# Kernel optimization log

Measured on AMD Instinct MI355X. Metric: run time of the kernel, lower is better.

Reference implementation:

```python
import jax, jax.numpy as jnp
import numpy as np

ITERS = 10  # resonator iterations (iterations=10 in init_kwargs)

def _bipolar(key, shape):
    return jnp.where(jax.random.normal(key, shape) >= 0, 1.0, -1.0).astype(jnp.float32)

def setup_inputs() -> dict:
    key = jax.random.key(0)
    k1, k2, k3 = jax.random.split(key, 3)
    b, f, v, d = 64, 4, 256, 16384
    input_ = _bipolar(k1, (b, d))
    init_estimates = _bipolar(k2, (b, f, d))
    codebooks = _bipolar(k3, (f, v, d))
    return {"input": input_, "init_estimates": init_estimates, "codebooks": codebooks}

def _sign(x):
    # multiset quantize: bipolar sign (ties -> +1), matching MAP-VSA quantization
    return jnp.where(x >= 0, 1.0, -1.0).astype(x.dtype)

def reference(input, init_estimates, codebooks):
    """CONCURRENT resonator, SOFTWARE mode, activation=NONE, stoch=NONE.
    input: (b, d) bipolar; init_estimates: (b, f, d); codebooks: (f, v, d).
    For bipolar vectors: bind = elementwise *, inverse = identity, so
    multibind of all-but-factor-j equals (product over all f) * estimate_j
    (since e*e = 1). This replaces the roll+stack+multibind with one fused pass.
    """
    def step(est, _):
        total = jnp.prod(est, axis=-2, keepdims=True)        # (b, 1, d)
        inv_others = total * est                             # (b, f, d) product of other factors
        new_est = input[:, None, :] * inv_others             # unbind: (b, f, d)
        sim = jnp.einsum('bfd,fvd->bfv', new_est, codebooks) # dot_similarity
        # multiset(codebook, similarity, quantize=True): sign of similarity-weighted sum
        est_new = _sign(jnp.einsum('bfv,fvd->bfd', sim, codebooks))
        return est_new, None
    est, _ = jax.lax.scan(step, init_estimates, None, length=ITERS)
    # cleanup: argmax of |similarity| per factor (argmax_abs=True)
    sim = jnp.einsum('bfd,fvd->bfv', est, codebooks)
    outcome = jnp.argmax(jnp.abs(sim), axis=-1)              # (b, f) codeword indices
    return est, outcome
```

## Files before the change

kernel.cpp:

```cpp
#include <hip/hip_runtime.h>
#include <stdint.h>

typedef unsigned long long ull;
typedef unsigned short ushort_t;
typedef __attribute__((ext_vector_type(8))) short bf16x8;
typedef __attribute__((ext_vector_type(4))) float f32x4;


__global__ __launch_bounds__(1024) void pack_mega(
        const float* __restrict__ in, const float* __restrict__ est_f,
        const float* __restrict__ cb,
        ull* __restrict__ in_bits, ull* __restrict__ est_bits, ull* __restrict__ cbw) {
    int wid  = (int)((blockIdx.x * 1024 + threadIdx.x) >> 6);
    int lane = threadIdx.x & 63;
    int w0 = wid * 16;
    const float* s;
    int wloc;
    if (w0 < 16384)      { s = in;    wloc = w0; }
    else if (w0 < 81920) { s = est_f; wloc = w0 - 16384; }
    else                 { s = cb;    wloc = w0 - 81920; }
    ull ball[16];
    #pragma unroll
    for (int k = 0; k < 16; ++k) {
        float x = s[(size_t)(wloc + k) * 64 + lane];
        ball[k] = __ballot(x < 0.0f);
    }
    if (lane == 0) {
        if (w0 < 16384) {
            #pragma unroll
            for (int k = 0; k < 16; ++k) in_bits[wloc + k] = ball[k];
        } else if (w0 < 81920) {
            #pragma unroll
            for (int k = 0; k < 16; ++k) est_bits[wloc + k] = ball[k];
        } else {
            #pragma unroll
            for (int k = 0; k < 16; ++k) {
                int g = wloc + k;
                int f = g >> 16, v = (g >> 8) & 255, w = g & 255;
                cbw[(size_t)(f * 256 + w) * 256 + v] = ball[k];
            }
        }
    }
}

__global__ __launch_bounds__(1024) void pack_cbT(const ull* __restrict__ cbw, ull* __restrict__ cbT) {
    int wid  = (int)((blockIdx.x * 1024 + threadIdx.x) >> 6);
    int lane = threadIdx.x & 63;
    int f = wid >> 12, j = (wid >> 10) & 3, w = (wid >> 2) & 255, s2 = wid & 3;
    ull cw = cbw[(size_t)(f * 256 + w) * 256 + j * 64 + lane];
    ull ball[16];
    #pragma unroll
    for (int k = 0; k < 16; ++k)
        ball[k] = __ballot((cw >> (s2 * 16 + k)) & 1ull);
    if (lane == 0) {
        #pragma unroll
        for (int k = 0; k < 16; ++k)
            cbT[(size_t)(f * 4 + j) * 16384 + w * 64 + s2 * 16 + k] = ball[k];
    }
}

__global__ __launch_bounds__(1024) void simA3_kernel(
        const ull* __restrict__ in_bits, const ull* __restrict__ est_in,
        const ull* __restrict__ cbw, ushort_t* __restrict__ outq, int mode) {
    int bid = blockIdx.x;
    int f    = (bid & 7) >> 1;
    int sub  = (bid & 1) * 32 + (bid >> 3);
    int vblk = sub & 3, bblk = sub >> 2;

    __shared__ ull s_cw[256][64];
    __shared__ ull s_ne[4][256];
    __shared__ short s_p[4][4][64];

    int t = threadIdx.x;

    {
        int bl = t >> 8, w = t & 255;
        int b = bblk * 4 + bl;
        ull e0 = est_in[(size_t)(b * 4 + 0) * 256 + w];
        ull e1 = est_in[(size_t)(b * 4 + 1) * 256 + w];
        ull e2 = est_in[(size_t)(b * 4 + 2) * 256 + w];
        ull e3 = est_in[(size_t)(b * 4 + 3) * 256 + w];
        ull ef = (f == 0) ? e0 : ((f == 1) ? e1 : ((f == 2) ? e2 : e3));
        s_ne[bl][w] = mode ? ef
                           : (in_bits[(size_t)b * 256 + w] ^ e0 ^ e1 ^ e2 ^ e3 ^ ef);
    }
    #pragma unroll 4
    for (int i = 0; i < 16; ++i) {
        int idx = i * 1024 + t;
        int w = idx >> 6, v = idx & 63;
        s_cw[w][v] = cbw[(size_t)(f * 256 + w) * 256 + vblk * 64 + v];
    }
    __syncthreads();

    {
        int lane = t & 63, wave = t >> 6;
        int bi = wave & 3, q = wave >> 2;
        int acc = 0;
        #pragma unroll 8
        for (int w = q * 64; w < q * 64 + 64; ++w)
            acc += __popcll(s_ne[bi][w] ^ s_cw[w][lane]);
        s_p[bi][q][lane] = (short)acc;
    }
    __syncthreads();

    if (t < 256) {
        int bi = t >> 6, v2 = t & 63;
        int h = s_p[bi][0][v2] + s_p[bi][1][v2] + s_p[bi][2][v2] + s_p[bi][3][v2];
        int b = bblk * 4 + bi, v = vblk * 64 + v2;
        if (mode == 0) {
            int sim = 16384 - 2 * h;
            int sh = sim >> 8, sl = sim & 255;
            size_t base = ((size_t)(f * 64 + b)) * 512 + v;
            outq[base]       = (ushort_t)(__float_as_uint((float)sh) >> 16);
            outq[base + 256] = (ushort_t)(__float_as_uint((float)sl) >> 16);
        } else {
            outq[((size_t)(f * 64 + b)) * 256 + v] = (ushort_t)(16384 - h);
        }
    }
}

__global__ __launch_bounds__(512) void gemm_kernel(
        const ull* __restrict__ cbT, const ushort_t* __restrict__ simAB,
        ull* __restrict__ est_out) {
    int bid = blockIdx.x;
    int fB   = (bid & 7) >> 1;
    int dblk = (bid & 1) * 32 + (bid >> 3);
    __shared__ int4 sB[8192];
    __shared__ ull s_ball[8][8][4];
    int t = threadIdx.x, lane = t & 63, wave = t >> 6;

    #pragma unroll 4
    for (int it = 0; it < 16; ++it) {
        int flat = it * 512 + t;
        int kc = flat >> 10, nt = (flat >> 6) & 15, l = flat & 63;
        int v0 = kc * 32 + ((l >> 4) << 3);
        int d  = dblk * 256 + nt * 16 + (l & 15);
        ull w = cbT[((size_t)fB * 4 + (v0 >> 6)) * 16384 + d];
        unsigned bits = (unsigned)(w >> (v0 & 63)) & 0xFFu;
        int4 val;
        val.x = 0x3F803F80 | ((bits & 1u) << 15)        | ((bits & 2u) << 30);
        val.y = 0x3F803F80 | (((bits >> 2) & 1u) << 15) | (((bits >> 2) & 2u) << 30);
        val.z = 0x3F803F80 | (((bits >> 4) & 1u) << 15) | (((bits >> 4) & 2u) << 30);
        val.w = 0x3F803F80 | (((bits >> 6) & 1u) << 15) | (((bits >> 6) & 2u) << 30);
        sB[flat] = val;
    }

    int mw = wave & 3, ntb = (wave >> 2) << 3;
    const ushort_t* abase = simAB
        + ((size_t)(fB * 64 + mw * 16 + (lane & 15))) * 512 + ((lane >> 4) << 3);
    bf16x8 Ahi[8], Alo[8];
    #pragma unroll
    for (int kc = 0; kc < 8; ++kc) {
        Ahi[kc] = *(const bf16x8*)(abase + kc * 32);
        Alo[kc] = *(const bf16x8*)(abase + 256 + kc * 32);
    }
    __syncthreads();

    #pragma unroll 2
    for (int ntl = 0; ntl < 8; ++ntl) {
        int nt = ntb + ntl;
        f32x4 acch = {0.f, 0.f, 0.f, 0.f}, accl = {0.f, 0.f, 0.f, 0.f};
        #pragma unroll
        for (int kc = 0; kc < 8; ++kc) {
            bf16x8 B = *(const bf16x8*)&sB[(kc * 16 + nt) * 64 + lane];
            acch = __builtin_amdgcn_mfma_f32_16x16x32_bf16(Ahi[kc], B, acch, 0, 0, 0);
            accl = __builtin_amdgcn_mfma_f32_16x16x32_bf16(Alo[kc], B, accl, 0, 0, 0);
        }
        #pragma unroll
        for (int r = 0; r < 4; ++r) {
            float S = 256.0f * acch[r] + accl[r];
            ull m = __ballot(S < 0.0f);
            if (lane == 0) s_ball[wave][nt & 7][r] = m;
        }
    }
    __syncthreads();

    if (t < 256) {
        int b = t >> 2, w4 = t & 3;
        int wv = (b >> 4) + ((w4 >= 2) ? 4 : 0);
        ull word = 0;
        #pragma unroll
        for (int k = 0; k < 4; ++k) {
            int nt = w4 * 4 + k;
            ull m = s_ball[wv][nt & 7][b & 3];
            word |= ((m >> (((b >> 2) & 3) * 16)) & 0xFFFFull) << (k * 16);
        }
        est_out[((size_t)(b * 4 + fB)) * 256 + dblk * 4 + w4] = word;
    }
}

__global__ __launch_bounds__(256) void final2_kernel(
        const ull* __restrict__ est, const ushort_t* __restrict__ simF,
        float* __restrict__ out) {
    int t = threadIdx.x;
    if (blockIdx.x < 256 && t < 64) {
        int b = blockIdx.x >> 2, f = blockIdx.x & 3;
        const ushort_t* sf = simF + ((size_t)(f * 64 + b)) * 256 + t * 4;
        int best_a = -1, best_v = 0;
        #pragma unroll
        for (int k = 0; k < 4; ++k) {
            int sim = 2 * (int)sf[k] - 16384;
            int a = sim < 0 ? -sim : sim;
            if (a > best_a) { best_a = a; best_v = t * 4 + k; }
        }
        #pragma unroll
        for (int off = 1; off < 64; off <<= 1) {
            int oa = __shfl_xor(best_a, off);
            int ov = __shfl_xor(best_v, off);
            if (oa > best_a || (oa == best_a && ov < best_v)) { best_a = oa; best_v = ov; }
        }
        if (t == 0) out[4194304 + b * 4 + f] = (float)best_v;
    }
    int flat = blockIdx.x * 2048 + t * 8;
    ull w = est[flat >> 6];
    unsigned bits = (unsigned)(w >> (flat & 63)) & 0xFFu;
    float4 lo, hi;
    lo.x = (bits & 1u)   ? -1.0f : 1.0f;
    lo.y = (bits & 2u)   ? -1.0f : 1.0f;
    lo.z = (bits & 4u)   ? -1.0f : 1.0f;
    lo.w = (bits & 8u)   ? -1.0f : 1.0f;
    hi.x = (bits & 16u)  ? -1.0f : 1.0f;
    hi.y = (bits & 32u)  ? -1.0f : 1.0f;
    hi.z = (bits & 64u)  ? -1.0f : 1.0f;
    hi.w = (bits & 128u) ? -1.0f : 1.0f;
    *(float4*)(out + flat)     = lo;
    *(float4*)(out + flat + 4) = hi;
}

extern "C" void kernel_launch(void* const* d_in, const int* in_sizes, int n_in,
                              void* d_out, int out_size, void* d_ws, size_t ws_size,
                              hipStream_t stream) {
    const float* input    = (const float*)d_in[0];
    const float* init_est = (const float*)d_in[1];
    const float* cb       = (const float*)d_in[2];
    float* out = (float*)d_out;
    char* ws = (char*)d_ws;

    ull* in_bits    = (ull*)(ws + 0);
    ull* est0       = (ull*)(ws + 131072);
    ull* est1       = (ull*)(ws + 655360);
    ull* cbw        = (ull*)(ws + 1179648);
    ull* cbT        = (ull*)(ws + 3276800);
    ushort_t* simAB = (ushort_t*)(ws + 5373952);
    ushort_t* simF  = simAB;

    pack_mega<<<1344, 1024, 0, stream>>>(input, init_est, cb, in_bits, est0, cbw);
    pack_cbT<<<1024, 1024, 0, stream>>>(cbw, cbT);

    ull* bufs[2] = { est0, est1 };
    for (int i = 0; i < 10; ++i) {
        simA3_kernel<<<256, 1024, 0, stream>>>(in_bits, bufs[i & 1], cbw, simAB, 0);
        gemm_kernel<<<256, 512, 0, stream>>>(cbT, simAB, bufs[(i & 1) ^ 1]);
    }
    simA3_kernel<<<256, 1024, 0, stream>>>(in_bits, est0, cbw, simF, 1);
    final2_kernel<<<2048, 256, 0, stream>>>(est0, simF, out);
}
```

Before: 318.9 us.

## Fuse resonator iterations into one persistent cooperative kernel with grid barriers

Replaces the 22 separate similarity/GEMM/final kernel launches with a single cooperative persistent kernel of 256 blocks. Blocks synchronise through atomic counters in global memory, and shared memory is reused between the popcount and MFMA phases. It also overlaps codebook staging into shared memory with the barrier waits. This removes launch overhead and inter-kernel gaps, at the cost of spin-wait barriers and reloading codebook tiles every iteration because the shared buffer is aliased.

```diff
diff --git a/kernel.cpp b/kernel.cpp
--- a/kernel.cpp
+++ b/kernel.cpp
@@ -2,15 +2,31 @@
 #include <stdint.h>
 
 typedef unsigned long long ull;
-typedef unsigned short ushort_t;
+typedef unsigned int u32;
 typedef __attribute__((ext_vector_type(8))) short bf16x8;
 typedef __attribute__((ext_vector_type(4))) float f32x4;
 
+
+#define AS __HIP_MEMORY_SCOPE_AGENT
+__device__ __forceinline__ ull ald(const ull* p) {
+    return __hip_atomic_load(p, __ATOMIC_RELAXED, AS);
+}
+__device__ __forceinline__ void ast(ull* p, ull v) {
+    __hip_atomic_store(p, v, __ATOMIC_RELAXED, AS);
+}
+__device__ __forceinline__ u32 ald32(const u32* p) {
+    return __hip_atomic_load(p, __ATOMIC_RELAXED, AS);
+}
+__device__ __forceinline__ void ast32(u32* p, u32 v) {
+    __hip_atomic_store(p, v, __ATOMIC_RELAXED, AS);
+}
 
 __global__ __launch_bounds__(1024) void pack_mega(
         const float* __restrict__ in, const float* __restrict__ est_f,
         const float* __restrict__ cb,
-        ull* __restrict__ in_bits, ull* __restrict__ est_bits, ull* __restrict__ cbw) {
+        ull* __restrict__ in_bits, ull* __restrict__ est_bits, ull* __restrict__ cbw,
+        ull* __restrict__ bar) {
+    if (blockIdx.x == 0 && threadIdx.x < 64) bar[threadIdx.x] = 0;
     int wid  = (int)((blockIdx.x * 1024 + threadIdx.x) >> 6);
     int lane = threadIdx.x & 63;
     int w0 = wid * 16;
@@ -59,147 +75,174 @@
     }
 }
 
-__global__ __launch_bounds__(1024) void simA3_kernel(
-        const ull* __restrict__ in_bits, const ull* __restrict__ est_in,
-        const ull* __restrict__ cbw, ushort_t* __restrict__ outq, int mode) {
+__global__ __launch_bounds__(512) void reso_kernel(
+        const ull* __restrict__ in_bits, ull* __restrict__ est0, ull* __restrict__ est1,
+        const ull* __restrict__ cbw, const ull* __restrict__ cbT,
+        u32* __restrict__ simAB, ull* __restrict__ bar, float* __restrict__ out) {
+    __shared__ __align__(16) char smraw[143360];
+    ull  (*s_cw)[64]     = (ull (*)[64])smraw;
+    ull  (*s_ne)[256]    = (ull (*)[256])(smraw + 131072);
+    short (*s_p)[8][64]  = (short (*)[8][64])(smraw + 139264);
+    int4* sB             = (int4*)smraw;
+    ull  (*s_ball)[8][4] = (ull (*)[8][4])(smraw + 131072);
+
+    int t = threadIdx.x, lane = t & 63, wave = t >> 6;
     int bid = blockIdx.x;
     int f    = (bid & 7) >> 1;
     int sub  = (bid & 1) * 32 + (bid >> 3);
     int vblk = sub & 3, bblk = sub >> 2;
-
-    __shared__ ull s_cw[256][64];
-    __shared__ ull s_ne[4][256];
-    __shared__ short s_p[4][4][64];
-
-    int t = threadIdx.x;
-
-    {
-        int bl = t >> 8, w = t & 255;
-        int b = bblk * 4 + bl;
-        ull e0 = est_in[(size_t)(b * 4 + 0) * 256 + w];
-        ull e1 = est_in[(size_t)(b * 4 + 1) * 256 + w];
-        ull e2 = est_in[(size_t)(b * 4 + 2) * 256 + w];
-        ull e3 = est_in[(size_t)(b * 4 + 3) * 256 + w];
-        ull ef = (f == 0) ? e0 : ((f == 1) ? e1 : ((f == 2) ? e2 : e3));
-        s_ne[bl][w] = mode ? ef
-                           : (in_bits[(size_t)b * 256 + w] ^ e0 ^ e1 ^ e2 ^ e3 ^ ef);
-    }
+    int dblk = sub;
+
     #pragma unroll 4
     for (int i = 0; i < 16; ++i) {
-        int idx = i * 1024 + t;
+        int idx = i * 1024 + t * 2;
         int w = idx >> 6, v = idx & 63;
-        s_cw[w][v] = cbw[(size_t)(f * 256 + w) * 256 + vblk * 64 + v];
-    }
-    __syncthreads();
-
-    {
-        int lane = t & 63, wave = t >> 6;
-        int bi = wave & 3, q = wave >> 2;
-        int acc = 0;
-        #pragma unroll 8
-        for (int w = q * 64; w < q * 64 + 64; ++w)
-            acc += __popcll(s_ne[bi][w] ^ s_cw[w][lane]);
-        s_p[bi][q][lane] = (short)acc;
-    }
-    __syncthreads();
-
-    if (t < 256) {
-        int bi = t >> 6, v2 = t & 63;
-        int h = s_p[bi][0][v2] + s_p[bi][1][v2] + s_p[bi][2][v2] + s_p[bi][3][v2];
-        int b = bblk * 4 + bi, v = vblk * 64 + v2;
-        if (mode == 0) {
-            int sim = 16384 - 2 * h;
-            int sh = sim >> 8, sl = sim & 255;
-            size_t base = ((size_t)(f * 64 + b)) * 512 + v;
-            outq[base]       = (ushort_t)(__float_as_uint((float)sh) >> 16);
-            outq[base + 256] = (ushort_t)(__float_as_uint((float)sl) >> 16);
-        } else {
-            outq[((size_t)(f * 64 + b)) * 256 + v] = (ushort_t)(16384 - h);
-        }
-    }
-}
-
-__global__ __launch_bounds__(512) void gemm_kernel(
-        const ull* __restrict__ cbT, const ushort_t* __restrict__ simAB,
-        ull* __restrict__ est_out) {
-    int bid = blockIdx.x;
-    int fB   = (bid & 7) >> 1;
-    int dblk = (bid & 1) * 32 + (bid >> 3);
-    __shared__ int4 sB[8192];
-    __shared__ ull s_ball[8][8][4];
-    int t = threadIdx.x, lane = t & 63, wave = t >> 6;
-
-    #pragma unroll 4
-    for (int it = 0; it < 16; ++it) {
-        int flat = it * 512 + t;
-        int kc = flat >> 10, nt = (flat >> 6) & 15, l = flat & 63;
-        int v0 = kc * 32 + ((l >> 4) << 3);
-        int d  = dblk * 256 + nt * 16 + (l & 15);
-        ull w = cbT[((size_t)fB * 4 + (v0 >> 6)) * 16384 + d];
-        unsigned bits = (unsigned)(w >> (v0 & 63)) & 0xFFu;
-        int4 val;
-        val.x = 0x3F803F80 | ((bits & 1u) << 15)        | ((bits & 2u) << 30);
-        val.y = 0x3F803F80 | (((bits >> 2) & 1u) << 15) | (((bits >> 2) & 2u) << 30);
-        val.z = 0x3F803F80 | (((bits >> 4) & 1u) << 15) | (((bits >> 4) & 2u) << 30);
-        val.w = 0x3F803F80 | (((bits >> 6) & 1u) << 15) | (((bits >> 6) & 2u) << 30);
-        sB[flat] = val;
-    }
-
-    int mw = wave & 3, ntb = (wave >> 2) << 3;
-    const ushort_t* abase = simAB
-        + ((size_t)(fB * 64 + mw * 16 + (lane & 15))) * 512 + ((lane >> 4) << 3);
-    bf16x8 Ahi[8], Alo[8];
-    #pragma unroll
-    for (int kc = 0; kc < 8; ++kc) {
-        Ahi[kc] = *(const bf16x8*)(abase + kc * 32);
-        Alo[kc] = *(const bf16x8*)(abase + 256 + kc * 32);
-    }
-    __syncthreads();
-
-    #pragma unroll 2
-    for (int ntl = 0; ntl < 8; ++ntl) {
-        int nt = ntb + ntl;
-        f32x4 acch = {0.f, 0.f, 0.f, 0.f}, accl = {0.f, 0.f, 0.f, 0.f};
+        *(ulonglong2*)&s_cw[w][v] =
+            *(const ulonglong2*)&cbw[(size_t)(f * 256 + w) * 256 + vblk * 64 + v];
+    }
+
+    for (int itr = 0; itr <= 10; ++itr) {
+        ull* estIn  = (itr & 1) ? est1 : est0;
+        ull* estOut = (itr & 1) ? est0 : est1;
+        const int mode = (itr == 10);
+
+        #pragma unroll
+        for (int i = 0; i < 2; ++i) {
+            int idx = i * 512 + t;
+            int bl = idx >> 8, w = idx & 255;
+            int b = bblk * 4 + bl;
+            ull e0 = ald(&estIn[(size_t)(b * 4 + 0) * 256 + w]);
+            ull e1 = ald(&estIn[(size_t)(b * 4 + 1) * 256 + w]);
+            ull e2 = ald(&estIn[(size_t)(b * 4 + 2) * 256 + w]);
+            ull e3 = ald(&estIn[(size_t)(b * 4 + 3) * 256 + w]);
+            ull ef = (f == 0) ? e0 : ((f == 1) ? e1 : ((f == 2) ? e2 : e3));
+            s_ne[bl][w] = mode ? ef : (in_bits[(size_t)b * 256 + w] ^ e0 ^ e1 ^ e2 ^ e3 ^ ef);
+        }
+        __syncthreads();
+        {
+            int acc0 = 0, acc1 = 0, acc2 = 0, acc3 = 0;
+            #pragma unroll 8
+            for (int w = wave * 32; w < wave * 32 + 32; ++w) {
+                ull cwv = s_cw[w][lane];
+                acc0 += __popcll(s_ne[0][w] ^ cwv);
+                acc1 += __popcll(s_ne[1][w] ^ cwv);
+                acc2 += __popcll(s_ne[2][w] ^ cwv);
+                acc3 += __popcll(s_ne[3][w] ^ cwv);
+            }
+            s_p[0][wave][lane] = (short)acc0;
+            s_p[1][wave][lane] = (short)acc1;
+            s_p[2][wave][lane] = (short)acc2;
+            s_p[3][wave][lane] = (short)acc3;
+        }
+        __syncthreads();
+        if (t < 256) {
+            int bi = t >> 6, v2 = t & 63;
+            int h = 0;
+            #pragma unroll
+            for (int c = 0; c < 8; ++c) h += s_p[bi][c][v2];
+            int b = bblk * 4 + bi, v = vblk * 64 + v2;
+            u32 val;
+            if (!mode) {
+                int sim = 16384 - 2 * h;
+                int sh = sim >> 8, sl = sim & 255;
+                val = (u32)(__float_as_uint((float)sh) >> 16)
+                    | ((u32)(__float_as_uint((float)sl) >> 16) << 16);
+            } else {
+                val = (u32)(16384 - h);
+            }
+            ast32(&simAB[((size_t)(f * 64 + b) << 8) + v], val);
+        }
+        __syncthreads();
+        if (t == 0) atomicAdd(&bar[itr * 2], 1ull);
+        if (!mode) {
+            #pragma unroll 4
+            for (int it2 = 0; it2 < 16; ++it2) {
+                int flat = it2 * 512 + t;
+                int kc = flat >> 10, nt = (flat >> 6) & 15, l = flat & 63;
+                int v0 = kc * 32 + ((l >> 4) << 3);
+                int d  = dblk * 256 + nt * 16 + (l & 15);
+                ull w = cbT[((size_t)f * 4 + (v0 >> 6)) * 16384 + d];
+                unsigned bits = (unsigned)(w >> (v0 & 63)) & 0xFFu;
+                int4 valB;
+                valB.x = 0x3F803F80 | ((bits & 1u) << 15)        | ((bits & 2u) << 30);
+                valB.y = 0x3F803F80 | (((bits >> 2) & 1u) << 15) | (((bits >> 2) & 2u) << 30);
+                valB.z = 0x3F803F80 | (((bits >> 4) & 1u) << 15) | (((bits >> 4) & 2u) << 30);
+                valB.w = 0x3F803F80 | (((bits >> 6) & 1u) << 15) | (((bits >> 6) & 2u) << 30);
+                sB[flat] = valB;
+            }
+        }
+        if (t == 0) { while (ald(&bar[itr * 2]) < 256ull) __builtin_amdgcn_s_sleep(1); }
+        __syncthreads();
+        if (mode) break;
+
+        int mw = wave & 3, ntb = (wave >> 2) << 3;
+        const ull* ab = (const ull*)(simAB + (((size_t)(f * 64 + mw * 16 + (lane & 15))) << 8))
+                        + ((lane >> 4) << 2);
+        bf16x8 Ahi[8], Alo[8];
         #pragma unroll
         for (int kc = 0; kc < 8; ++kc) {
-            bf16x8 B = *(const bf16x8*)&sB[(kc * 16 + nt) * 64 + lane];
-            acch = __builtin_amdgcn_mfma_f32_16x16x32_bf16(Ahi[kc], B, acch, 0, 0, 0);
-            accl = __builtin_amdgcn_mfma_f32_16x16x32_bf16(Alo[kc], B, accl, 0, 0, 0);
-        }
-        #pragma unroll
-        for (int r = 0; r < 4; ++r) {
-            float S = 256.0f * acch[r] + accl[r];
-            ull m = __ballot(S < 0.0f);
-            if (lane == 0) s_ball[wave][nt & 7][r] = m;
-        }
-    }
-    __syncthreads();
-
-    if (t < 256) {
-        int b = t >> 2, w4 = t & 3;
-        int wv = (b >> 4) + ((w4 >= 2) ? 4 : 0);
-        ull word = 0;
+            union { u32 u[4]; bf16x8 v; } H, L;
+            #pragma unroll
+            for (int p2 = 0; p2 < 4; ++p2) {
+                ull w = ald(ab + kc * 16 + p2);
+                H.u[p2] = (u32)(w & 0xFFFFull) | (((u32)(w >> 32) & 0xFFFFu) << 16);
+                L.u[p2] = ((u32)(w >> 16) & 0xFFFFu) | ((u32)(w >> 48) << 16);
+            }
+            Ahi[kc] = H.v; Alo[kc] = L.v;
+        }
+        #pragma unroll 2
+        for (int ntl = 0; ntl < 8; ++ntl) {
+            int nt = ntb + ntl;
+            f32x4 acch = {0.f, 0.f, 0.f, 0.f}, accl = {0.f, 0.f, 0.f, 0.f};
+            #pragma unroll
+            for (int kc = 0; kc < 8; ++kc) {
+                bf16x8 B = *(const bf16x8*)&sB[(kc * 16 + nt) * 64 + lane];
+                acch = __builtin_amdgcn_mfma_f32_16x16x32_bf16(Ahi[kc], B, acch, 0, 0, 0);
+                accl = __builtin_amdgcn_mfma_f32_16x16x32_bf16(Alo[kc], B, accl, 0, 0, 0);
+            }
+            #pragma unroll
+            for (int r = 0; r < 4; ++r) {
+                float S = 256.0f * acch[r] + accl[r];
+                ull m = __ballot(S < 0.0f);
+                if (lane == 0) s_ball[wave][nt & 7][r] = m;
+            }
+        }
+        __syncthreads();
+        if (t < 256) {
+            int b = t >> 2, w4 = t & 3;
+            int wv = (b >> 4) + ((w4 >= 2) ? 4 : 0);
+            ull word = 0;
+            #pragma unroll
+            for (int k = 0; k < 4; ++k) {
+                int nt = w4 * 4 + k;
+                ull m = s_ball[wv][nt & 7][b & 3];
+                word |= ((m >> (((b >> 2) & 3) * 16)) & 0xFFFFull) << (k * 16);
+            }
+            ast(&estOut[((size_t)(b * 4 + f)) * 256 + dblk * 4 + w4], word);
+        }
+        __syncthreads();
+        if (t == 0) atomicAdd(&bar[itr * 2 + 1], 1ull);
+        #pragma unroll 4
+        for (int i = 0; i < 16; ++i) {
+            int idx = i * 1024 + t * 2;
+            int w = idx >> 6, v = idx & 63;
+            *(ulonglong2*)&s_cw[w][v] =
+                *(const ulonglong2*)&cbw[(size_t)(f * 256 + w) * 256 + vblk * 64 + v];
+        }
+        if (t == 0) { while (ald(&bar[itr * 2 + 1]) < 256ull) __builtin_amdgcn_s_sleep(1); }
+        __syncthreads();
+    }
+
+    if (t < 64) {
+        int b2 = bid >> 2, f2 = bid & 3;
+        const ull* sf = (const ull*)(simAB + ((size_t)(f2 * 64 + b2) << 8)) + t * 2;
+        ull w0 = ald(sf), w1 = ald(sf + 1);
+        int qv[4] = { (int)(u32)w0, (int)(u32)(w0 >> 32),
+                      (int)(u32)w1, (int)(u32)(w1 >> 32) };
+        int best_a = -1, best_v = 0;
         #pragma unroll
         for (int k = 0; k < 4; ++k) {
-            int nt = w4 * 4 + k;
-            ull m = s_ball[wv][nt & 7][b & 3];
-            word |= ((m >> (((b >> 2) & 3) * 16)) & 0xFFFFull) << (k * 16);
-        }
-        est_out[((size_t)(b * 4 + fB)) * 256 + dblk * 4 + w4] = word;
-    }
-}
-
-__global__ __launch_bounds__(256) void final2_kernel(
-        const ull* __restrict__ est, const ushort_t* __restrict__ simF,
-        float* __restrict__ out) {
-    int t = threadIdx.x;
-    if (blockIdx.x < 256 && t < 64) {
-        int b = blockIdx.x >> 2, f = blockIdx.x & 3;
-        const ushort_t* sf = simF + ((size_t)(f * 64 + b)) * 256 + t * 4;
-        int best_a = -1, best_v = 0;
-        #pragma unroll
-        for (int k = 0; k < 4; ++k) {
-            int sim = 2 * (int)sf[k] - 16384;
+            int sim = 2 * qv[k] - 16384;
             int a = sim < 0 ? -sim : sim;
             if (a > best_a) { best_a = a; best_v = t * 4 + k; }
         }
@@ -209,22 +252,23 @@
             int ov = __shfl_xor(best_v, off);
             if (oa > best_a || (oa == best_a && ov < best_v)) { best_a = oa; best_v = ov; }
         }
-        if (t == 0) out[4194304 + b * 4 + f] = (float)best_v;
-    }
-    int flat = blockIdx.x * 2048 + t * 8;
-    ull w = est[flat >> 6];
-    unsigned bits = (unsigned)(w >> (flat & 63)) & 0xFFu;
-    float4 lo, hi;
-    lo.x = (bits & 1u)   ? -1.0f : 1.0f;
-    lo.y = (bits & 2u)   ? -1.0f : 1.0f;
-    lo.z = (bits & 4u)   ? -1.0f : 1.0f;
-    lo.w = (bits & 8u)   ? -1.0f : 1.0f;
-    hi.x = (bits & 16u)  ? -1.0f : 1.0f;
-    hi.y = (bits & 32u)  ? -1.0f : 1.0f;
-    hi.z = (bits & 64u)  ? -1.0f : 1.0f;
-    hi.w = (bits & 128u) ? -1.0f : 1.0f;
-    *(float4*)(out + flat)     = lo;
-    *(float4*)(out + flat + 4) = hi;
+        if (t == 0) out[4194304 + b2 * 4 + f2] = (float)best_v;
+    }
+    {
+        int widx = bid * 256 + (t >> 1);
+        ull w = ald(&est0[widx]);
+        u32 bits = (u32)(w >> ((t & 1) * 32));
+        int base = bid * 16384 + (t >> 1) * 64 + (t & 1) * 32;
+        #pragma unroll
+        for (int j = 0; j < 8; ++j) {
+            float4 o;
+            o.x = ((bits >> (j * 4 + 0)) & 1u) ? -1.0f : 1.0f;
+            o.y = ((bits >> (j * 4 + 1)) & 1u) ? -1.0f : 1.0f;
+            o.z = ((bits >> (j * 4 + 2)) & 1u) ? -1.0f : 1.0f;
+            o.w = ((bits >> (j * 4 + 3)) & 1u) ? -1.0f : 1.0f;
+            *(float4*)(out + base + j * 4) = o;
+        }
+    }
 }
 
 extern "C" void kernel_launch(void* const* d_in, const int* in_sizes, int n_in,
@@ -236,22 +280,21 @@
     float* out = (float*)d_out;
     char* ws = (char*)d_ws;
 
-    ull* in_bits    = (ull*)(ws + 0);
-    ull* est0       = (ull*)(ws + 131072);
-    ull* est1       = (ull*)(ws + 655360);
-    ull* cbw        = (ull*)(ws + 1179648);
-    ull* cbT        = (ull*)(ws + 3276800);
-    ushort_t* simAB = (ushort_t*)(ws + 5373952);
-    ushort_t* simF  = simAB;
-
-    pack_mega<<<1344, 1024, 0, stream>>>(input, init_est, cb, in_bits, est0, cbw);
+    ull* in_bits = (ull*)(ws + 0);
+    ull* est0    = (ull*)(ws + 131072);
+    ull* est1    = (ull*)(ws + 655360);
+    ull* cbw     = (ull*)(ws + 1179648);
+    ull* cbT     = (ull*)(ws + 3276800);
+    u32* simAB   = (u32*)(ws + 5373952);
+    ull* bar     = (ull*)(ws + 5636096);
+
+    pack_mega<<<1344, 1024, 0, stream>>>(input, init_est, cb, in_bits, est0, cbw, bar);
     pack_cbT<<<1024, 1024, 0, stream>>>(cbw, cbT);
 
-    ull* bufs[2] = { est0, est1 };
-    for (int i = 0; i < 10; ++i) {
-        simA3_kernel<<<256, 1024, 0, stream>>>(in_bits, bufs[i & 1], cbw, simAB, 0);
-        gemm_kernel<<<256, 512, 0, stream>>>(cbT, simAB, bufs[(i & 1) ^ 1]);
-    }
-    simA3_kernel<<<256, 1024, 0, stream>>>(in_bits, est0, cbw, simF, 1);
-    final2_kernel<<<2048, 256, 0, stream>>>(est0, simF, out);
-}
+    void* kargs[] = {
+        (void*)&in_bits, (void*)&est0, (void*)&est1, (void*)&cbw, (void*)&cbT,
+        (void*)&simAB, (void*)&bar, (void*)&out
+    };
+    hipLaunchCooperativeKernel(reinterpret_cast<void*>(reso_kernel),
+                               dim3(256, 1, 1), dim3(512, 1, 1), kargs, 0, stream);
+}
```

After: 391.6 us. +22.8%, slower.

## Register-resident popcount similarity and on-the-fly bf16 B expansion in GEMM

Applied to the files above, without the earlier changes.

The similarity kernel no longer stages the codebook and unbound estimates in shared memory. Each wave keeps 16 codebook words in registers and broadcasts estimate words with readlane, so the popcounts are split across 16 waves per block. The GEMM now stages only the packed bit codebook (8 KB) in LDS and expands bits to bf16 ±1 right before each MFMA, replacing the 128 KB pre-expanded tile. The hi/lo similarity outputs are written interleaved in an MFMA-fragment order so A-operand loads are coalesced; the cost is extra ALU work for unpacking inside the inner loop.

```diff
diff --git a/kernel.cpp b/kernel.cpp
--- a/kernel.cpp
+++ b/kernel.cpp
@@ -2,6 +2,7 @@
 #include <stdint.h>
 
 typedef unsigned long long ull;
+typedef unsigned int u32;
 typedef unsigned short ushort_t;
 typedef __attribute__((ext_vector_type(8))) short bf16x8;
 typedef __attribute__((ext_vector_type(4))) float f32x4;
@@ -59,100 +60,97 @@
     }
 }
 
-__global__ __launch_bounds__(1024) void simA3_kernel(
+__global__ __launch_bounds__(1024) void simA4_kernel(
         const ull* __restrict__ in_bits, const ull* __restrict__ est_in,
-        const ull* __restrict__ cbw, ushort_t* __restrict__ outq, int mode) {
+        const ull* __restrict__ cbw, u32* __restrict__ simAB, int mode) {
+    __shared__ short s_p[4][16][64];
+    int t = threadIdx.x, lane = t & 63, wave = t >> 6;
     int bid = blockIdx.x;
     int f    = (bid & 7) >> 1;
     int sub  = (bid & 1) * 32 + (bid >> 3);
     int vblk = sub & 3, bblk = sub >> 2;
 
-    __shared__ ull s_cw[256][64];
-    __shared__ ull s_ne[4][256];
-    __shared__ short s_p[4][4][64];
-
-    int t = threadIdx.x;
-
-    {
-        int bl = t >> 8, w = t & 255;
-        int b = bblk * 4 + bl;
-        ull e0 = est_in[(size_t)(b * 4 + 0) * 256 + w];
-        ull e1 = est_in[(size_t)(b * 4 + 1) * 256 + w];
-        ull e2 = est_in[(size_t)(b * 4 + 2) * 256 + w];
-        ull e3 = est_in[(size_t)(b * 4 + 3) * 256 + w];
-        ull ef = (f == 0) ? e0 : ((f == 1) ? e1 : ((f == 2) ? e2 : e3));
-        s_ne[bl][w] = mode ? ef
-                           : (in_bits[(size_t)b * 256 + w] ^ e0 ^ e1 ^ e2 ^ e3 ^ ef);
-    }
-    #pragma unroll 4
-    for (int i = 0; i < 16; ++i) {
-        int idx = i * 1024 + t;
-        int w = idx >> 6, v = idx & 63;
-        s_cw[w][v] = cbw[(size_t)(f * 256 + w) * 256 + vblk * 64 + v];
-    }
-    __syncthreads();
-
-    {
-        int lane = t & 63, wave = t >> 6;
-        int bi = wave & 3, q = wave >> 2;
-        int acc = 0;
-        #pragma unroll 8
-        for (int w = q * 64; w < q * 64 + 64; ++w)
-            acc += __popcll(s_ne[bi][w] ^ s_cw[w][lane]);
-        s_p[bi][q][lane] = (short)acc;
-    }
+    int bA = bblk * 4 + (lane >> 4);
+    int wA = wave * 16 + (lane & 15);
+    ull e0 = est_in[(size_t)(bA * 4 + 0) * 256 + wA];
+    ull e1 = est_in[(size_t)(bA * 4 + 1) * 256 + wA];
+    ull e2 = est_in[(size_t)(bA * 4 + 2) * 256 + wA];
+    ull e3 = est_in[(size_t)(bA * 4 + 3) * 256 + wA];
+    ull ef = (f == 0) ? e0 : ((f == 1) ? e1 : ((f == 2) ? e2 : e3));
+    ull ne = mode ? ef : (in_bits[(size_t)bA * 256 + wA] ^ e0 ^ e1 ^ e2 ^ e3 ^ ef);
+    u32 ne_lo = (u32)ne, ne_hi = (u32)(ne >> 32);
+
+    ull cw[16];
+    const ull* cbase = cbw + (size_t)(f * 256 + wave * 16) * 256 + vblk * 64 + lane;
+    #pragma unroll
+    for (int k = 0; k < 16; ++k) cw[k] = cbase[(size_t)k * 256];
+
+    int acc0 = 0, acc1 = 0, acc2 = 0, acc3 = 0;
+    #pragma unroll
+    for (int k = 0; k < 16; ++k) {
+        u32 cl = (u32)cw[k], ch = (u32)(cw[k] >> 32);
+        #pragma unroll
+        for (int bi = 0; bi < 4; ++bi) {
+            u32 a0 = __builtin_amdgcn_readlane(ne_lo, bi * 16 + k);
+            u32 a1 = __builtin_amdgcn_readlane(ne_hi, bi * 16 + k);
+            int p = __builtin_popcount(cl ^ a0) + __builtin_popcount(ch ^ a1);
+            if (bi == 0) acc0 += p; else if (bi == 1) acc1 += p;
+            else if (bi == 2) acc2 += p; else acc3 += p;
+        }
+    }
+    s_p[0][wave][lane] = (short)acc0;
+    s_p[1][wave][lane] = (short)acc1;
+    s_p[2][wave][lane] = (short)acc2;
+    s_p[3][wave][lane] = (short)acc3;
     __syncthreads();
 
     if (t < 256) {
         int bi = t >> 6, v2 = t & 63;
-        int h = s_p[bi][0][v2] + s_p[bi][1][v2] + s_p[bi][2][v2] + s_p[bi][3][v2];
+        int h = 0;
+        #pragma unroll
+        for (int q = 0; q < 16; ++q) h += s_p[bi][q][v2];
         int b = bblk * 4 + bi, v = vblk * 64 + v2;
-        if (mode == 0) {
+        if (!mode) {
             int sim = 16384 - 2 * h;
             int sh = sim >> 8, sl = sim & 255;
-            size_t base = ((size_t)(f * 64 + b)) * 512 + v;
-            outq[base]       = (ushort_t)(__float_as_uint((float)sh) >> 16);
-            outq[base + 256] = (ushort_t)(__float_as_uint((float)sl) >> 16);
+            u32 val = (u32)(__float_as_uint((float)sh) >> 16)
+                    | ((u32)(__float_as_uint((float)sl) >> 16) << 16);
+            int mw = b >> 4, brow = b & 15;
+            int kc = v >> 5, kgrp = (v >> 3) & 3, j = v & 7;
+            int uidx = ((((mw * 8 + kc) * 4 + (j >> 1)) * 64) + kgrp * 16 + brow) * 2 + (j & 1);
+            simAB[f * 16384 + uidx] = val;
         } else {
-            outq[((size_t)(f * 64 + b)) * 256 + v] = (ushort_t)(16384 - h);
-        }
-    }
-}
-
-__global__ __launch_bounds__(512) void gemm_kernel(
-        const ull* __restrict__ cbT, const ushort_t* __restrict__ simAB,
+            simAB[((f * 64 + b) << 8) + v] = (u32)(16384 - h);
+        }
+    }
+}
+
+__global__ __launch_bounds__(512) void gemm4_kernel(
+        const ull* __restrict__ cbT, const u32* __restrict__ simAB,
         ull* __restrict__ est_out) {
     int bid = blockIdx.x;
     int fB   = (bid & 7) >> 1;
     int dblk = (bid & 1) * 32 + (bid >> 3);
-    __shared__ int4 sB[8192];
+    __shared__ ull s_bT[1024];
     __shared__ ull s_ball[8][8][4];
     int t = threadIdx.x, lane = t & 63, wave = t >> 6;
 
-    #pragma unroll 4
-    for (int it = 0; it < 16; ++it) {
-        int flat = it * 512 + t;
-        int kc = flat >> 10, nt = (flat >> 6) & 15, l = flat & 63;
-        int v0 = kc * 32 + ((l >> 4) << 3);
-        int d  = dblk * 256 + nt * 16 + (l & 15);
-        ull w = cbT[((size_t)fB * 4 + (v0 >> 6)) * 16384 + d];
-        unsigned bits = (unsigned)(w >> (v0 & 63)) & 0xFFu;
-        int4 val;
-        val.x = 0x3F803F80 | ((bits & 1u) << 15)        | ((bits & 2u) << 30);
-        val.y = 0x3F803F80 | (((bits >> 2) & 1u) << 15) | (((bits >> 2) & 2u) << 30);
-        val.z = 0x3F803F80 | (((bits >> 4) & 1u) << 15) | (((bits >> 4) & 2u) << 30);
-        val.w = 0x3F803F80 | (((bits >> 6) & 1u) << 15) | (((bits >> 6) & 2u) << 30);
-        sB[flat] = val;
-    }
+    s_bT[t]       = cbT[((size_t)fB * 4 + (t >> 8)) * 16384 + dblk * 256 + (t & 255)];
+    s_bT[t + 512] = cbT[((size_t)fB * 4 + ((t + 512) >> 8)) * 16384 + dblk * 256 + (t & 255)];
 
     int mw = wave & 3, ntb = (wave >> 2) << 3;
-    const ushort_t* abase = simAB
-        + ((size_t)(fB * 64 + mw * 16 + (lane & 15))) * 512 + ((lane >> 4) << 3);
+    const ull* ab8 = (const ull*)simAB + (size_t)fB * 8192;
     bf16x8 Ahi[8], Alo[8];
     #pragma unroll
     for (int kc = 0; kc < 8; ++kc) {
-        Ahi[kc] = *(const bf16x8*)(abase + kc * 32);
-        Alo[kc] = *(const bf16x8*)(abase + 256 + kc * 32);
+        union { u32 u[4]; bf16x8 v; } H, L;
+        #pragma unroll
+        for (int n = 0; n < 4; ++n) {
+            ull w = ab8[(((mw * 8 + kc) * 4 + n) * 64) + lane];
+            H.u[n] = (u32)(w & 0xFFFFull) | (((u32)(w >> 32) & 0xFFFFu) << 16);
+            L.u[n] = ((u32)(w >> 16) & 0xFFFFu) | ((u32)(w >> 48) << 16);
+        }
+        Ahi[kc] = H.v; Alo[kc] = L.v;
     }
     __syncthreads();
 
@@ -162,15 +160,21 @@
         f32x4 acch = {0.f, 0.f, 0.f, 0.f}, accl = {0.f, 0.f, 0.f, 0.f};
         #pragma unroll
         for (int kc = 0; kc < 8; ++kc) {
-            bf16x8 B = *(const bf16x8*)&sB[(kc * 16 + nt) * 64 + lane];
-            acch = __builtin_amdgcn_mfma_f32_16x16x32_bf16(Ahi[kc], B, acch, 0, 0, 0);
-            accl = __builtin_amdgcn_mfma_f32_16x16x32_bf16(Alo[kc], B, accl, 0, 0, 0);
+            ull w = s_bT[(kc >> 1) * 256 + nt * 16 + (lane & 15)];
+            u32 bits = (u32)(w >> ((kc & 1) * 32 + (lane >> 4) * 8)) & 0xFFu;
+            union { u32 u[4]; bf16x8 v; } B;
+            B.u[0] = 0x3F803F80 | ((bits & 1u) << 15)        | ((bits & 2u) << 30);
+            B.u[1] = 0x3F803F80 | (((bits >> 2) & 1u) << 15) | (((bits >> 2) & 2u) << 30);
+            B.u[2] = 0x3F803F80 | (((bits >> 4) & 1u) << 15) | (((bits >> 4) & 2u) << 30);
+            B.u[3] = 0x3F803F80 | (((bits >> 6) & 1u) << 15) | (((bits >> 6) & 2u) << 30);
+            acch = __builtin_amdgcn_mfma_f32_16x16x32_bf16(Ahi[kc], B.v, acch, 0, 0, 0);
+            accl = __builtin_amdgcn_mfma_f32_16x16x32_bf16(Alo[kc], B.v, accl, 0, 0, 0);
         }
         #pragma unroll
         for (int r = 0; r < 4; ++r) {
             float S = 256.0f * acch[r] + accl[r];
             ull m = __ballot(S < 0.0f);
-            if (lane == 0) s_ball[wave][nt & 7][r] = m;
+            if (lane == 0) s_ball[wave][ntl][r] = m;
         }
     }
     __syncthreads();
@@ -190,12 +194,12 @@
 }
 
 __global__ __launch_bounds__(256) void final2_kernel(
-        const ull* __restrict__ est, const ushort_t* __restrict__ simF,
+        const ull* __restrict__ est, const u32* __restrict__ simF,
         float* __restrict__ out) {
     int t = threadIdx.x;
     if (blockIdx.x < 256 && t < 64) {
         int b = blockIdx.x >> 2, f = blockIdx.x & 3;
-        const ushort_t* sf = simF + ((size_t)(f * 64 + b)) * 256 + t * 4;
+        const u32* sf = simF + ((size_t)(f * 64 + b) << 8) + t * 4;
         int best_a = -1, best_v = 0;
         #pragma unroll
         for (int k = 0; k < 4; ++k) {
@@ -236,22 +240,21 @@
     float* out = (float*)d_out;
     char* ws = (char*)d_ws;
 
-    ull* in_bits    = (ull*)(ws + 0);
-    ull* est0       = (ull*)(ws + 131072);
-    ull* est1       = (ull*)(ws + 655360);
-    ull* cbw        = (ull*)(ws + 1179648);
-    ull* cbT        = (ull*)(ws + 3276800);
-    ushort_t* simAB = (ushort_t*)(ws + 5373952);
-    ushort_t* simF  = simAB;
+    ull* in_bits = (ull*)(ws + 0);
+    ull* est0    = (ull*)(ws + 131072);
+    ull* est1    = (ull*)(ws + 655360);
+    ull* cbw     = (ull*)(ws + 1179648);
+    ull* cbT     = (ull*)(ws + 3276800);
+    u32* simAB   = (u32*)(ws + 5373952);
 
     pack_mega<<<1344, 1024, 0, stream>>>(input, init_est, cb, in_bits, est0, cbw);
     pack_cbT<<<1024, 1024, 0, stream>>>(cbw, cbT);
 
     ull* bufs[2] = { est0, est1 };
     for (int i = 0; i < 10; ++i) {
-        simA3_kernel<<<256, 1024, 0, stream>>>(in_bits, bufs[i & 1], cbw, simAB, 0);
-        gemm_kernel<<<256, 512, 0, stream>>>(cbT, simAB, bufs[(i & 1) ^ 1]);
-    }
-    simA3_kernel<<<256, 1024, 0, stream>>>(in_bits, est0, cbw, simF, 1);
-    final2_kernel<<<2048, 256, 0, stream>>>(est0, simF, out);
-}
+        simA4_kernel<<<256, 1024, 0, stream>>>(in_bits, bufs[i & 1], cbw, simAB, 0);
+        gemm4_kernel<<<256, 512, 0, stream>>>(cbT, simAB, bufs[(i & 1) ^ 1]);
+    }
+    simA4_kernel<<<256, 1024, 0, stream>>>(in_bits, est0, cbw, simAB, 1);
+    final2_kernel<<<2048, 256, 0, stream>>>(est0, simAB, out);
+}
```

Measured after the change: 314.3 us. About the same (-1.5%).
